# Kernel tuning notes

Measured on AMD Instinct MI355X. Metric: run time of the kernel, lower is better.

The kernel has to match this reference:

```python
import jax, jax.numpy as jnp
import numpy as np

N = 100000
E = 1600000
F_IN = 100
HID = 128
CLS = 47


def _glorot(key, shape):
    fan_in, fan_out = shape[1], shape[0]
    lim = (6.0 / (fan_in + fan_out)) ** 0.5
    return jax.random.uniform(key, shape, jnp.float32, -lim, lim)


def setup_inputs() -> dict:
    key = jax.random.key(0)
    ks = jax.random.split(key, 12)
    x0 = jax.random.normal(ks[0], (N, F_IN), jnp.float32)
    edge_index = jax.random.randint(ks[1], (2, E), 0, N, jnp.int32)
    edge_weight = jax.random.uniform(ks[2], (E,), jnp.float32)
    params = {
        'W1_rel': _glorot(ks[3], (HID, F_IN)),
        'W1_root': _glorot(ks[4], (HID, F_IN)),
        'b1': jnp.zeros((HID,), jnp.float32),
        'W2_rel': _glorot(ks[5], (HID, HID)),
        'W2_root': _glorot(ks[6], (HID, HID)),
        'b2': jnp.zeros((HID,), jnp.float32),
        'W3_rel': _glorot(ks[7], (HID, HID)),
        'W3_root': _glorot(ks[8], (HID, HID)),
        'b3': jnp.zeros((HID,), jnp.float32),
        'W_lin': _glorot(ks[9], (CLS, 3 * HID)),
        'b_lin': jnp.zeros((CLS,), jnp.float32),
    }
    return dict(x0=x0, edge_index=edge_index, edge_weight=edge_weight, **params)


def _graph_conv(x, src, dst, ew, W_rel, W_root, b):
    # gather source features, scale by edge weight, scatter-add to destinations
    msg = x[src] * ew[:, None]                       # [E, d]
    agg = jax.ops.segment_sum(msg, dst, num_segments=N)  # [N, d]
    return agg @ W_rel.T + x @ W_root.T + b


def reference(x0, edge_index, edge_weight,
              W1_rel, W1_root, b1,
              W2_rel, W2_root, b2,
              W3_rel, W3_root, b3,
              W_lin, b_lin):
    src, dst = edge_index[0], edge_index[1]
    x1 = jax.nn.relu(_graph_conv(x0, src, dst, edge_weight, W1_rel, W1_root, b1))
    x2 = jax.nn.relu(_graph_conv(x1, src, dst, edge_weight, W2_rel, W2_root, b2))
    x3 = jax.nn.relu(_graph_conv(x2, src, dst, edge_weight, W3_rel, W3_root, b3))
    x = jnp.concatenate([x1, x2, x3], axis=-1)       # [N, 3*HID]
    logits = x @ W_lin.T + b_lin                     # [N, CLS]
    return jax.nn.log_softmax(logits, axis=-1)
```

## Files before the change

### kernel.cpp

```cpp
#include <hip/hip_runtime.h>
#include <hip/hip_bf16.h>
#include <stdint.h>

#define NN 100000
#define NE 1600000
#define FIN 100
#define HID 128
#define CLS 47
#define NBUK 391

typedef __attribute__((ext_vector_type(8))) short bf16x8;
typedef __attribute__((ext_vector_type(4))) float f32x4;
typedef __attribute__((ext_vector_type(2))) float f32x2;

#define AS1(p) ((const __attribute__((address_space(1))) void*)(p))
#define AS3(p) ((__attribute__((address_space(3))) void*)(p))

__device__ __forceinline__ uint16_t f2bf(float f) {
  union { float f; uint32_t u; } v; v.f = f;
  uint32_t r = v.u + 0x7fffu + ((v.u >> 16) & 1u);
  return (uint16_t)(r >> 16);
}

__global__ void pack_weights(const float* __restrict__ W1r, const float* __restrict__ W1o,
                             const float* __restrict__ W2r, const float* __restrict__ W2o,
                             const float* __restrict__ W3r, const float* __restrict__ W3o,
                             uint16_t* __restrict__ B1, uint16_t* __restrict__ B2, uint16_t* __restrict__ B3) {
  int idx = blockIdx.x * 256 + threadIdx.x;
  int l = idx >> 15;
  int rem = idx & 32767;
  int j = rem >> 8;
  int k = rem & 255;
  if (l == 0) {
    uint16_t v = 0;
    if (k < FIN) v = f2bf(W1r[j*FIN + k]);
    else if (k >= 128 && k < 128 + FIN) v = f2bf(W1o[j*FIN + (k - 128)]);
    B1[j*256 + k] = v;
  } else if (l == 1) {
    B2[j*256 + k] = (k < 128) ? f2bf(W2r[j*128 + k]) : f2bf(W2o[j*128 + (k - 128)]);
  } else {
    B3[j*256 + k] = (k < 128) ? f2bf(W3r[j*128 + k]) : f2bf(W3o[j*128 + (k - 128)]);
  }
}

__global__ void pack_wl(const float* __restrict__ Wl, uint16_t* __restrict__ Wlb) {
  int idx = blockIdx.x * 256 + threadIdx.x;
  int r = idx / 384;
  int c = idx - r * 384;
  Wlb[idx] = (r < CLS) ? f2bf(Wl[r*384 + c]) : (uint16_t)0;
}

__global__ __launch_bounds__(256) void pad_x0(const float* __restrict__ x0, uint16_t* __restrict__ x0p,
                                              uint8_t* __restrict__ x0f8) {
  int n = blockIdx.x * 4 + (threadIdx.x >> 6);
  int c = 2 * (threadIdx.x & 63);
  uint32_t o = 0;
  uint16_t o8 = 0;
  if (c < FIN) {
    float2 v = *(const float2*)(x0 + (size_t)n*FIN + c);
    o = ((uint32_t)f2bf(v.y) << 16) | (uint32_t)f2bf(v.x);
    o8 = (uint16_t)__builtin_amdgcn_cvt_pk_fp8_f32(v.x, v.y, 0, false);
  }
  *(uint32_t*)(x0p + (size_t)n*HID + c) = o;
  *(uint16_t*)(x0f8 + (size_t)n*128 + c) = o8;
}

__global__ __launch_bounds__(512) void bucket_hist(const int* __restrict__ dst, int* __restrict__ bcnt) {
  __shared__ int h[NBUK];
  int tid = threadIdx.x;
  for (int i = tid; i < NBUK; i += 512) h[i] = 0;
  __syncthreads();
  int tile0 = blockIdx.x * 8192;
  int n = NE - tile0; if (n > 8192) n = 8192;
  for (int i = tid; i < n; i += 512) atomicAdd(&h[dst[tile0 + i] >> 8], 1);
  __syncthreads();
  for (int i = tid; i < NBUK; i += 512) if (h[i]) atomicAdd(&bcnt[i], h[i]);
}

__global__ __launch_bounds__(512) void bucket_scan(const int* __restrict__ bcnt,
                                                   int* __restrict__ bfill, int* __restrict__ bbase) {
  __shared__ int sh[512];
  int t = threadIdx.x;
  int v = (t < NBUK) ? bcnt[t] : 0;
  sh[t] = v;
  __syncthreads();
  for (int off = 1; off < 512; off <<= 1) {
    int tv = (t >= off) ? sh[t - off] : 0;
    __syncthreads();
    sh[t] += tv;
    __syncthreads();
  }
  if (t < NBUK) {
    int e = sh[t] - v;
    bfill[t] = e;
    bbase[t] = e;
  }
  if (t == 0) bbase[NBUK] = NE;
}

__global__ __launch_bounds__(512) void binscat(const int* __restrict__ src, const int* __restrict__ dst,
                                               const float* __restrict__ ew,
                                               int* __restrict__ bfill, int2* __restrict__ ebin) {
  __shared__ int h[NBUK];
  __shared__ int base[NBUK];
  int tid = threadIdx.x;
  for (int i = tid; i < NBUK; i += 512) h[i] = 0;
  __syncthreads();
  int tile0 = blockIdx.x * 8192;
  int n = NE - tile0; if (n > 8192) n = 8192;
  for (int i = tid; i < n; i += 512) atomicAdd(&h[dst[tile0 + i] >> 8], 1);
  __syncthreads();
  for (int i = tid; i < NBUK; i += 512) base[i] = h[i] ? atomicAdd(&bfill[i], h[i]) : 0;
  __syncthreads();
  for (int i = tid; i < NBUK; i += 512) h[i] = 0;
  __syncthreads();
  for (int i = tid; i < n; i += 512) {
    int e = tile0 + i;
    int d = dst[e];
    int b = d >> 8;
    int r = atomicAdd(&h[b], 1);
    ebin[base[b] + r] = make_int2(src[e] | ((d & 255) << 17), __float_as_int(ew[e]));
  }
}

__global__ __launch_bounds__(256) void bucket_csr(const int2* __restrict__ ebin,
                                                  const int* __restrict__ bbase,
                                                  int* __restrict__ row_start,
                                                  int2* __restrict__ erec) {
  __shared__ int sh[256];
  __shared__ int fill[256];
  int b = blockIdx.x;
  int tid = threadIdx.x;
  int ebase = bbase[b], eend = bbase[b + 1];
  int cnt = eend - ebase;
  sh[tid] = 0;
  __syncthreads();
  for (int i = tid; i < cnt; i += 256) atomicAdd(&sh[(uint32_t)ebin[ebase + i].x >> 17], 1);
  __syncthreads();
  int histv = sh[tid];
  __syncthreads();
  for (int off = 1; off < 256; off <<= 1) {
    int tv = (tid >= off) ? sh[tid - off] : 0;
    __syncthreads();
    sh[tid] += tv;
    __syncthreads();
  }
  int excl = sh[tid] - histv;
  int node = b * 256 + tid;
  if (node <= NN) row_start[node] = ebase + excl;
  fill[tid] = ebase + excl;
  __syncthreads();
  for (int i = tid; i < cnt; i += 256) {
    int2 rec = ebin[ebase + i];
    int dl = (uint32_t)rec.x >> 17;
    int s = rec.x & 0x1FFFF;
    int pos = atomicAdd(&fill[dl], 1);
    erec[pos] = make_int2(s << 7, rec.y);
  }
}

__global__ __launch_bounds__(256) void spmm_kernel(const uint8_t* __restrict__ x8,
                                                   const int* __restrict__ row_start,
                                                   const int2* __restrict__ erec,
                                                   uint16_t* __restrict__ agg) {
  int wave = threadIdx.x >> 6;
  int l = threadIdx.x & 63;
  int half = l >> 5, li = l & 31;
  int n = blockIdx.x * 8 + wave * 2 + half;
  int s0 = row_start[n], s1 = row_start[n + 1];
  const char* xb = (const char*)x8;
  int loff = 4 * li;
  f32x2 a01 = (f32x2){0.f, 0.f}, a23 = (f32x2){0.f, 0.f};
  const int2* ep = erec + s0;
  int deg = s1 - s0;
  int nfull = deg & ~15;
  const int2* epf = ep + nfull;
  for (; ep < epf; ep += 16) {
    int2 r[16];
    #pragma unroll
    for (int u = 0; u < 16; ++u) r[u] = ep[u];
    uint32_t g[16];
    #pragma unroll
    for (int u = 0; u < 16; ++u)
      g[u] = *(const uint32_t*)(xb + (size_t)(uint32_t)(r[u].x + loff));
    #pragma unroll
    for (int u = 0; u < 16; ++u) {
      float w = __int_as_float(r[u].y);
      f32x2 w2 = (f32x2){w, w};
      a01 += w2 * __builtin_amdgcn_cvt_pk_f32_fp8(g[u], false);
      a23 += w2 * __builtin_amdgcn_cvt_pk_f32_fp8(g[u], true);
    }
  }
  int rem = deg - nfull;
  if (rem) {
    int2 r[16];
    #pragma unroll
    for (int u = 0; u < 16; ++u) r[u] = ep[u];
    uint32_t g[16];
    #pragma unroll
    for (int u = 0; u < 16; ++u)
      g[u] = *(const uint32_t*)(xb + (size_t)(uint32_t)(r[u].x + loff));
    #pragma unroll
    for (int u = 0; u < 16; ++u) {
      float w = (u < rem) ? __int_as_float(r[u].y) : 0.f;
      f32x2 w2 = (f32x2){w, w};
      a01 += w2 * __builtin_amdgcn_cvt_pk_f32_fp8(g[u], false);
      a23 += w2 * __builtin_amdgcn_cvt_pk_f32_fp8(g[u], true);
    }
  }
  uint2 o;
  o.x = ((uint32_t)f2bf(a01[1]) << 16) | (uint32_t)f2bf(a01[0]);
  o.y = ((uint32_t)f2bf(a23[1]) << 16) | (uint32_t)f2bf(a23[0]);
  *(uint2*)(agg + (size_t)n*HID + 4*li) = o;
}

__global__ __launch_bounds__(256) void gemm_kernel(const uint16_t* __restrict__ A1, const uint16_t* __restrict__ A2,
                                                   const uint16_t* __restrict__ Bm, const float* __restrict__ bias,
                                                   uint16_t* __restrict__ out, uint8_t* __restrict__ out8) {
  __shared__ uint16_t ldsA[128 * 32];
  __shared__ uint16_t ldsB[128 * 32];
  int t = threadIdx.x;
  int n0 = blockIdx.x * 128;
  int lane = t & 63, wave = t >> 6;
  int wm = (wave >> 1) * 64, wn = (wave & 1) * 64;
  int l15 = lane & 15, quad = lane >> 4;

  f32x4 acc[4][4];
  #pragma unroll
  for (int i = 0; i < 4; ++i)
    #pragma unroll
    for (int j = 0; j < 4; ++j) acc[i][j] = (f32x4){0.f, 0.f, 0.f, 0.f};

  for (int kt = 0; kt < 8; ++kt) {
    int kbase = kt * 32;
    const uint16_t* Asrc = (kbase < 128) ? A1 : A2;
    int klocal = kbase & 127;
    #pragma unroll
    for (int q = 0; q < 2; ++q) {
      int u = t + q * 256;
      int r = u >> 2;
      int kg = (u & 3) * 8;
      int rowA = n0 + r; if (rowA >= NN) rowA = NN - 1;
      __builtin_amdgcn_global_load_lds(AS1(Asrc + (size_t)rowA*HID + klocal + kg), AS3(&ldsA[u * 8]), 16, 0, 0);
      __builtin_amdgcn_global_load_lds(AS1(Bm + r*256 + kbase + kg), AS3(&ldsB[u * 8]), 16, 0, 0);
    }
    __syncthreads();
    bf16x8 af[4], bfr[4];
    #pragma unroll
    for (int mi = 0; mi < 4; ++mi) af[mi] = *(const bf16x8*)&ldsA[(wm + mi*16 + l15) * 32 + quad * 8];
    #pragma unroll
    for (int ni = 0; ni < 4; ++ni) bfr[ni] = *(const bf16x8*)&ldsB[(wn + ni*16 + l15) * 32 + quad * 8];
    #pragma unroll
    for (int mi = 0; mi < 4; ++mi)
      #pragma unroll
      for (int ni = 0; ni < 4; ++ni)
        acc[mi][ni] = __builtin_amdgcn_mfma_f32_16x16x32_bf16(af[mi], bfr[ni], acc[mi][ni], 0, 0, 0);
    __syncthreads();
  }

  #pragma unroll
  for (int mi = 0; mi < 4; ++mi) {
    #pragma unroll
    for (int ni = 0; ni < 4; ++ni) {
      int c = wn + ni*16 + l15;
      float bc = bias[c];
      #pragma unroll
      for (int i = 0; i < 4; ++i) {
        int r = n0 + wm + mi*16 + quad*4 + i;
        if (r < NN) {
          float v = acc[mi][ni][i] + bc;
          v = v > 0.f ? v : 0.f;
          out[(size_t)r*HID + c] = f2bf(v);
          if (out8) out8[(size_t)r*128 + c] = (uint8_t)__builtin_amdgcn_cvt_pk_fp8_f32(v, v, 0, false);
        }
      }
    }
  }
}

__global__ __launch_bounds__(256) void final_kernel(const uint16_t* __restrict__ x1, const uint16_t* __restrict__ x2,
                                                    const uint16_t* __restrict__ x3,
                                                    const uint16_t* __restrict__ Wlb, const float* __restrict__ bl,
                                                    float* __restrict__ out) {
  __shared__ uint16_t ldsA[4 * 64 * 8];
  __shared__ uint16_t ldsW[4 * 64 * 8];
  int t = threadIdx.x;
  int lane = t & 63, wave = t >> 6;
  int n0 = blockIdx.x * 64;
  int l15 = lane & 15, quad = lane >> 4;

  int sc2 = t >> 6, sr = t & 63;
  int rowA = n0 + sr; if (rowA >= NN) rowA = NN - 1;
  int rowW = sr < 48 ? sr : 47;

  f32x4 acc[3];
  #pragma unroll
  for (int i = 0; i < 3; ++i) acc[i] = (f32x4){0.f, 0.f, 0.f, 0.f};

  #pragma unroll
  for (int kt = 0; kt < 12; ++kt) {
    const uint16_t* xs = (kt < 4) ? x1 : (kt < 8) ? x2 : x3;
    int klocal = (kt & 3) * 32 + sc2 * 8;
    __builtin_amdgcn_global_load_lds(AS1(xs + (size_t)rowA*HID + klocal), AS3(&ldsA[t * 8]), 16, 0, 0);
    __builtin_amdgcn_global_load_lds(AS1(Wlb + (size_t)rowW*384 + kt*32 + sc2*8), AS3(&ldsW[t * 8]), 16, 0, 0);
    __syncthreads();
    bf16x8 af = *(const bf16x8*)&ldsA[(quad * 64 + wave * 16 + l15) * 8];
    #pragma unroll
    for (int nt = 0; nt < 3; ++nt) {
      bf16x8 wf = *(const bf16x8*)&ldsW[(quad * 64 + nt * 16 + l15) * 8];
      acc[nt] = __builtin_amdgcn_mfma_f32_16x16x32_bf16(af, wf, acc[nt], 0, 0, 0);
    }
    __syncthreads();
  }

  int nb = n0 + wave * 16;
  float bias[3]; bool valid[3];
  #pragma unroll
  for (int nt = 0; nt < 3; ++nt) {
    int c = nt*16 + l15;
    valid[nt] = (c < CLS);
    bias[nt] = valid[nt] ? bl[c] : 0.f;
  }

  #pragma unroll
  for (int i = 0; i < 4; ++i) {
    int r = nb + quad*4 + i;
    float v0 = acc[0][i] + bias[0];
    float v1 = acc[1][i] + bias[1];
    float v2 = valid[2] ? (acc[2][i] + bias[2]) : -INFINITY;
    float m = fmaxf(v0, fmaxf(v1, v2));
    #pragma unroll
    for (int off = 8; off >= 1; off >>= 1) m = fmaxf(m, __shfl_xor(m, off, 64));
    float s = __expf(v0 - m) + __expf(v1 - m) + (valid[2] ? __expf(v2 - m) : 0.f);
    #pragma unroll
    for (int off = 8; off >= 1; off >>= 1) s += __shfl_xor(s, off, 64);
    float lse = m + __logf(s);
    if (r < NN) {
      out[(size_t)r*CLS + l15]      = v0 - lse;
      out[(size_t)r*CLS + 16 + l15] = v1 - lse;
      if (valid[2]) out[(size_t)r*CLS + 32 + l15] = v2 - lse;
    }
  }
}

extern "C" void kernel_launch(void* const* d_in, const int* in_sizes, int n_in,
                              void* d_out, int out_size, void* d_ws, size_t ws_size,
                              hipStream_t stream) {
  (void)in_sizes; (void)n_in; (void)out_size; (void)ws_size;
  const float* x0  = (const float*)d_in[0];
  const int*   ei  = (const int*)d_in[1];
  const float* ew  = (const float*)d_in[2];
  const float* W1r = (const float*)d_in[3];
  const float* W1o = (const float*)d_in[4];
  const float* b1  = (const float*)d_in[5];
  const float* W2r = (const float*)d_in[6];
  const float* W2o = (const float*)d_in[7];
  const float* b2  = (const float*)d_in[8];
  const float* W3r = (const float*)d_in[9];
  const float* W3o = (const float*)d_in[10];
  const float* b3  = (const float*)d_in[11];
  const float* Wl  = (const float*)d_in[12];
  const float* bl  = (const float*)d_in[13];
  const int* src = ei;
  const int* dst = ei + NE;

  char* ws = (char*)d_ws;
  size_t off = 0;
  auto alloc = [&](size_t bytes) -> void* {
    void* p = ws + off;
    off += (bytes + 255) & ~(size_t)255;
    return p;
  };
  uint16_t* x0p = (uint16_t*)alloc((size_t)NN * HID * 2);
  uint16_t* xb1 = (uint16_t*)alloc((size_t)NN * HID * 2);
  uint16_t* xb3 = (uint16_t*)alloc((size_t)NN * HID * 2);
  uint16_t* agg = (uint16_t*)alloc((size_t)NN * HID * 2);
  int2*   erec      = (int2*)alloc((size_t)(NE + 16) * 8);
  int2*   ebin      = (int2*)alloc((size_t)NE * 8);
  int*    row_start = (int*)alloc((size_t)(NN + 1) * 4);
  int*    bcnt      = (int*)alloc(NBUK * 4);
  int*    bfill     = (int*)alloc(NBUK * 4);
  int*    bbase     = (int*)alloc((NBUK + 1) * 4);
  uint16_t* B1 = (uint16_t*)alloc(128 * 256 * 2);
  uint16_t* B2 = (uint16_t*)alloc(128 * 256 * 2);
  uint16_t* B3 = (uint16_t*)alloc(128 * 256 * 2);
  uint16_t* Wlb = (uint16_t*)alloc(48 * 384 * 2);
  uint8_t* x0f8  = (uint8_t*)alloc((size_t)NN * 128);
  uint8_t* xb2f8 = (uint8_t*)alloc((size_t)NN * 128);
  uint16_t* xb2 = x0p;
  uint8_t* xb1f8 = (uint8_t*)ebin;

  const int TB = (NE + 8191) / 8192;

  hipMemsetAsync(bcnt, 0, NBUK * 4, stream);
  hipMemsetAsync(erec + NE, 0, 16 * sizeof(int2), stream);
  pack_weights<<<384, 256, 0, stream>>>(W1r, W1o, W2r, W2o, W3r, W3o, B1, B2, B3);
  pack_wl<<<72, 256, 0, stream>>>(Wl, Wlb);
  pad_x0<<<NN / 4, 256, 0, stream>>>(x0, x0p, x0f8);
  bucket_hist<<<TB, 512, 0, stream>>>(dst, bcnt);
  bucket_scan<<<1, 512, 0, stream>>>(bcnt, bfill, bbase);
  binscat<<<TB, 512, 0, stream>>>(src, dst, ew, bfill, ebin);
  bucket_csr<<<NBUK, 256, 0, stream>>>(ebin, bbase, row_start, erec);

  spmm_kernel<<<NN / 8, 256, 0, stream>>>(x0f8, row_start, erec, agg);
  gemm_kernel<<<(NN + 127) / 128, 256, 0, stream>>>(agg, x0p, B1, b1, xb1, xb1f8);
  spmm_kernel<<<NN / 8, 256, 0, stream>>>(xb1f8, row_start, erec, agg);
  gemm_kernel<<<(NN + 127) / 128, 256, 0, stream>>>(agg, xb1, B2, b2, xb2, xb2f8);
  spmm_kernel<<<NN / 8, 256, 0, stream>>>(xb2f8, row_start, erec, agg);
  gemm_kernel<<<(NN + 127) / 128, 256, 0, stream>>>(agg, xb2, B3, b3, xb3, nullptr);

  final_kernel<<<(NN + 63) / 64, 256, 0, stream>>>(xb1, xb2, xb3, Wlb, bl, (float*)d_out);
}
```

Baseline: 411.3 us.

## Use fixed-capacity edge buckets, drop histogram/scan passes, restage final GEMM loads

Result: faster. 394.5 us (-4.1%).

```diff
diff --git a/kernel.cpp b/kernel.cpp
--- a/kernel.cpp
+++ b/kernel.cpp
@@ -8,6 +8,7 @@
 #define HID 128
 #define CLS 47
 #define NBUK 391
+#define BCAP 4608
 
 typedef __attribute__((ext_vector_type(8))) short bf16x8;
 typedef __attribute__((ext_vector_type(4))) float f32x4;
@@ -65,37 +66,9 @@
   *(uint16_t*)(x0f8 + (size_t)n*128 + c) = o8;
 }
 
-__global__ __launch_bounds__(512) void bucket_hist(const int* __restrict__ dst, int* __restrict__ bcnt) {
-  __shared__ int h[NBUK];
-  int tid = threadIdx.x;
-  for (int i = tid; i < NBUK; i += 512) h[i] = 0;
-  __syncthreads();
-  int tile0 = blockIdx.x * 8192;
-  int n = NE - tile0; if (n > 8192) n = 8192;
-  for (int i = tid; i < n; i += 512) atomicAdd(&h[dst[tile0 + i] >> 8], 1);
-  __syncthreads();
-  for (int i = tid; i < NBUK; i += 512) if (h[i]) atomicAdd(&bcnt[i], h[i]);
-}
-
-__global__ __launch_bounds__(512) void bucket_scan(const int* __restrict__ bcnt,
-                                                   int* __restrict__ bfill, int* __restrict__ bbase) {
-  __shared__ int sh[512];
-  int t = threadIdx.x;
-  int v = (t < NBUK) ? bcnt[t] : 0;
-  sh[t] = v;
-  __syncthreads();
-  for (int off = 1; off < 512; off <<= 1) {
-    int tv = (t >= off) ? sh[t - off] : 0;
-    __syncthreads();
-    sh[t] += tv;
-    __syncthreads();
-  }
-  if (t < NBUK) {
-    int e = sh[t] - v;
-    bfill[t] = e;
-    bbase[t] = e;
-  }
-  if (t == 0) bbase[NBUK] = NE;
+__global__ void binit(int* __restrict__ bfill) {
+  int i = blockIdx.x * 256 + threadIdx.x;
+  if (i < NBUK) bfill[i] = i * BCAP;
 }
 
 __global__ __launch_bounds__(512) void binscat(const int* __restrict__ src, const int* __restrict__ dst,
@@ -124,18 +97,18 @@
 }
 
 __global__ __launch_bounds__(256) void bucket_csr(const int2* __restrict__ ebin,
-                                                  const int* __restrict__ bbase,
-                                                  int* __restrict__ row_start,
+                                                  const int* __restrict__ bfill,
+                                                  int2* __restrict__ row_desc,
                                                   int2* __restrict__ erec) {
   __shared__ int sh[256];
   __shared__ int fill[256];
   int b = blockIdx.x;
   int tid = threadIdx.x;
-  int ebase = bbase[b], eend = bbase[b + 1];
-  int cnt = eend - ebase;
+  int base = b * BCAP;
+  int cnt = bfill[b] - base;
   sh[tid] = 0;
   __syncthreads();
-  for (int i = tid; i < cnt; i += 256) atomicAdd(&sh[(uint32_t)ebin[ebase + i].x >> 17], 1);
+  for (int i = tid; i < cnt; i += 256) atomicAdd(&sh[(uint32_t)ebin[base + i].x >> 17], 1);
   __syncthreads();
   int histv = sh[tid];
   __syncthreads();
@@ -147,32 +120,36 @@
   }
   int excl = sh[tid] - histv;
   int node = b * 256 + tid;
-  if (node <= NN) row_start[node] = ebase + excl;
-  fill[tid] = ebase + excl;
+  if (node < NN) row_desc[node] = make_int2(base + excl, histv);
+  fill[tid] = base + excl;
   __syncthreads();
   for (int i = tid; i < cnt; i += 256) {
-    int2 rec = ebin[ebase + i];
+    int2 rec = ebin[base + i];
     int dl = (uint32_t)rec.x >> 17;
     int s = rec.x & 0x1FFFF;
     int pos = atomicAdd(&fill[dl], 1);
     erec[pos] = make_int2(s << 7, rec.y);
   }
+  if (tid < 16) {
+    int p = cnt + tid;
+    if (p < BCAP) erec[base + p] = make_int2(0, 0);
+  }
 }
 
 __global__ __launch_bounds__(256) void spmm_kernel(const uint8_t* __restrict__ x8,
-                                                   const int* __restrict__ row_start,
+                                                   const int2* __restrict__ row_desc,
                                                    const int2* __restrict__ erec,
                                                    uint16_t* __restrict__ agg) {
   int wave = threadIdx.x >> 6;
   int l = threadIdx.x & 63;
   int half = l >> 5, li = l & 31;
   int n = blockIdx.x * 8 + wave * 2 + half;
-  int s0 = row_start[n], s1 = row_start[n + 1];
+  int2 rd = row_desc[n];
+  int s0 = rd.x, deg = rd.y;
   const char* xb = (const char*)x8;
   int loff = 4 * li;
   f32x2 a01 = (f32x2){0.f, 0.f}, a23 = (f32x2){0.f, 0.f};
   const int2* ep = erec + s0;
-  int deg = s1 - s0;
   int nfull = deg & ~15;
   const int2* epf = ep + nfull;
   for (; ep < epf; ep += 16) {
@@ -183,6 +160,7 @@
     #pragma unroll
     for (int u = 0; u < 16; ++u)
       g[u] = *(const uint32_t*)(xb + (size_t)(uint32_t)(r[u].x + loff));
+    __builtin_amdgcn_sched_barrier(0);
     #pragma unroll
     for (int u = 0; u < 16; ++u) {
       float w = __int_as_float(r[u].y);
@@ -200,6 +178,7 @@
     #pragma unroll
     for (int u = 0; u < 16; ++u)
       g[u] = *(const uint32_t*)(xb + (size_t)(uint32_t)(r[u].x + loff));
+    __builtin_amdgcn_sched_barrier(0);
     #pragma unroll
     for (int u = 0; u < 16; ++u) {
       float w = (u < rem) ? __int_as_float(r[u].y) : 0.f;
@@ -282,33 +261,42 @@
                                                     const uint16_t* __restrict__ x3,
                                                     const uint16_t* __restrict__ Wlb, const float* __restrict__ bl,
                                                     float* __restrict__ out) {
-  __shared__ uint16_t ldsA[4 * 64 * 8];
-  __shared__ uint16_t ldsW[4 * 64 * 8];
+  __shared__ uint16_t ldsA[64 * 16 * 8];
+  __shared__ uint16_t ldsW[64 * 16 * 8];
   int t = threadIdx.x;
   int lane = t & 63, wave = t >> 6;
   int n0 = blockIdx.x * 64;
   int l15 = lane & 15, quad = lane >> 4;
 
-  int sc2 = t >> 6, sr = t & 63;
-  int rowA = n0 + sr; if (rowA >= NN) rowA = NN - 1;
-  int rowW = sr < 48 ? sr : 47;
-
   f32x4 acc[3];
   #pragma unroll
   for (int i = 0; i < 3; ++i) acc[i] = (f32x4){0.f, 0.f, 0.f, 0.f};
 
   #pragma unroll
-  for (int kt = 0; kt < 12; ++kt) {
-    const uint16_t* xs = (kt < 4) ? x1 : (kt < 8) ? x2 : x3;
-    int klocal = (kt & 3) * 32 + sc2 * 8;
-    __builtin_amdgcn_global_load_lds(AS1(xs + (size_t)rowA*HID + klocal), AS3(&ldsA[t * 8]), 16, 0, 0);
-    __builtin_amdgcn_global_load_lds(AS1(Wlb + (size_t)rowW*384 + kt*32 + sc2*8), AS3(&ldsW[t * 8]), 16, 0, 0);
-    __syncthreads();
-    bf16x8 af = *(const bf16x8*)&ldsA[(quad * 64 + wave * 16 + l15) * 8];
-    #pragma unroll
-    for (int nt = 0; nt < 3; ++nt) {
-      bf16x8 wf = *(const bf16x8*)&ldsW[(quad * 64 + nt * 16 + l15) * 8];
-      acc[nt] = __builtin_amdgcn_mfma_f32_16x16x32_bf16(af, wf, acc[nt], 0, 0, 0);
+  for (int rr = 0; rr < 3; ++rr) {
+    const uint16_t* xs = (rr == 0) ? x1 : (rr == 1) ? x2 : x3;
+    #pragma unroll
+    for (int q = 0; q < 4; ++q) {
+      int u = t + q * 256;
+      int row = u >> 4, cp = u & 15;
+      int c = cp ^ (row & 15);
+      int rowA = n0 + row; if (rowA >= NN) rowA = NN - 1;
+      __builtin_amdgcn_global_load_lds(AS1(xs + (size_t)rowA*HID + c*8), AS3(&ldsA[u * 8]), 16, 0, 0);
+      int rowW = row < 48 ? row : 47;
+      __builtin_amdgcn_global_load_lds(AS1(Wlb + (size_t)rowW*384 + rr*128 + c*8), AS3(&ldsW[u * 8]), 16, 0, 0);
+    }
+    __syncthreads();
+    #pragma unroll
+    for (int kt = 0; kt < 4; ++kt) {
+      int cA = kt * 4 + quad;
+      int rA = wave * 16 + l15;
+      bf16x8 af = *(const bf16x8*)&ldsA[(rA * 16 + (cA ^ (rA & 15))) * 8];
+      #pragma unroll
+      for (int nt = 0; nt < 3; ++nt) {
+        int rW = nt * 16 + l15;
+        bf16x8 wf = *(const bf16x8*)&ldsW[(rW * 16 + (cA ^ (rW & 15))) * 8];
+        acc[nt] = __builtin_amdgcn_mfma_f32_16x16x32_bf16(af, wf, acc[nt], 0, 0, 0);
+      }
     }
     __syncthreads();
   }
@@ -375,12 +363,10 @@
   uint16_t* xb1 = (uint16_t*)alloc((size_t)NN * HID * 2);
   uint16_t* xb3 = (uint16_t*)alloc((size_t)NN * HID * 2);
   uint16_t* agg = (uint16_t*)alloc((size_t)NN * HID * 2);
-  int2*   erec      = (int2*)alloc((size_t)(NE + 16) * 8);
-  int2*   ebin      = (int2*)alloc((size_t)NE * 8);
-  int*    row_start = (int*)alloc((size_t)(NN + 1) * 4);
-  int*    bcnt      = (int*)alloc(NBUK * 4);
+  int2*   erec      = (int2*)alloc((size_t)NBUK * BCAP * 8);
+  int2*   ebin      = (int2*)alloc((size_t)NBUK * BCAP * 8);
+  int2*   row_desc  = (int2*)alloc((size_t)NN * 8);
   int*    bfill     = (int*)alloc(NBUK * 4);
-  int*    bbase     = (int*)alloc((NBUK + 1) * 4);
   uint16_t* B1 = (uint16_t*)alloc(128 * 256 * 2);
   uint16_t* B2 = (uint16_t*)alloc(128 * 256 * 2);
   uint16_t* B3 = (uint16_t*)alloc(128 * 256 * 2);
@@ -392,21 +378,18 @@
 
   const int TB = (NE + 8191) / 8192;
 
-  hipMemsetAsync(bcnt, 0, NBUK * 4, stream);
-  hipMemsetAsync(erec + NE, 0, 16 * sizeof(int2), stream);
+  binit<<<2, 256, 0, stream>>>(bfill);
   pack_weights<<<384, 256, 0, stream>>>(W1r, W1o, W2r, W2o, W3r, W3o, B1, B2, B3);
   pack_wl<<<72, 256, 0, stream>>>(Wl, Wlb);
   pad_x0<<<NN / 4, 256, 0, stream>>>(x0, x0p, x0f8);
-  bucket_hist<<<TB, 512, 0, stream>>>(dst, bcnt);
-  bucket_scan<<<1, 512, 0, stream>>>(bcnt, bfill, bbase);
   binscat<<<TB, 512, 0, stream>>>(src, dst, ew, bfill, ebin);
-  bucket_csr<<<NBUK, 256, 0, stream>>>(ebin, bbase, row_start, erec);
-
-  spmm_kernel<<<NN / 8, 256, 0, stream>>>(x0f8, row_start, erec, agg);
+  bucket_csr<<<NBUK, 256, 0, stream>>>(ebin, bfill, row_desc, erec);
+
+  spmm_kernel<<<NN / 8, 256, 0, stream>>>(x0f8, row_desc, erec, agg);
   gemm_kernel<<<(NN + 127) / 128, 256, 0, stream>>>(agg, x0p, B1, b1, xb1, xb1f8);
-  spmm_kernel<<<NN / 8, 256, 0, stream>>>(xb1f8, row_start, erec, agg);
+  spmm_kernel<<<NN / 8, 256, 0, stream>>>(xb1f8, row_desc, erec, agg);
   gemm_kernel<<<(NN + 127) / 128, 256, 0, stream>>>(agg, xb1, B2, b2, xb2, xb2f8);
-  spmm_kernel<<<NN / 8, 256, 0, stream>>>(xb2f8, row_start, erec, agg);
+  spmm_kernel<<<NN / 8, 256, 0, stream>>>(xb2f8, row_desc, erec, agg);
   gemm_kernel<<<(NN + 127) / 128, 256, 0, stream>>>(agg, xb2, B3, b3, xb3, nullptr);
 
   final_kernel<<<(NN + 63) / 64, 256, 0, stream>>>(xb1, xb2, xb3, Wlb, bl, (float*)d_out);
```
